# Optimization experiments

Hardware: AMD Instinct MI355X
Metric: run time of the kernel (lower is better)

## Reference

```python
import jax, jax.numpy as jnp
import numpy as np

CODEBOOK_SIZE = 8192
TOKEN_SIZE = 256
COMMITMENT_COST = 0.25


def setup_inputs() -> dict:
    key = jax.random.key(0)
    k1, k2 = jax.random.split(key)
    z = jax.random.normal(k1, (32, 1024, TOKEN_SIZE), dtype=jnp.float32)
    # embedding initialized uniform in [-1/K, 1/K] as in torch module
    embedding = jax.random.uniform(
        k2, (CODEBOOK_SIZE, TOKEN_SIZE), dtype=jnp.float32,
        minval=-1.0 / CODEBOOK_SIZE, maxval=1.0 / CODEBOOK_SIZE)
    return {"z": z, "embedding": embedding}


def reference(z, embedding):
    B, T, D = z.shape
    zf = z.reshape(B * T, D)                               # [N, D]
    # squared euclidean distances: ||z||^2 + ||e||^2 - 2 z.e
    d = (jnp.sum(zf * zf, axis=1, keepdims=True)
         + jnp.sum(embedding * embedding, axis=1)
         - 2.0 * jnp.einsum('nd,kd->nk', zf, embedding))   # [N, K]
    idx = jnp.argmin(d, axis=1)                            # [N]
    z_q = embedding[idx].reshape(B, T, D)                  # codebook gather
    commitment_loss = COMMITMENT_COST * jnp.mean(
        (jax.lax.stop_gradient(z_q) - z) ** 2)
    codebook_loss = jnp.mean((z_q - jax.lax.stop_gradient(z)) ** 2)
    loss = commitment_loss + codebook_loss                 # ema_update=False
    # straight-through estimator
    z_q_st = z + jax.lax.stop_gradient(z_q - z)
    return (z_q_st, loss, commitment_loss, codebook_loss,
            idx.reshape(B, T))
```

## Files before the change

kernel.cpp:

```cpp
#include <hip/hip_runtime.h>
#include <cfloat>

#define N_TOK   32768
#define K_CODES 8192
#define D_DIM   256
#define BTOK    128
#define CHUNK   128
#define NSPLIT  4
#define SPLITK  (K_CODES / NSPLIT)
#define CTAU_M  3.0e-5f
#define CAND_MM 2.4e-5f
#define MAXCAND 16
#define RBTOK   32
#define NRS     8
#define RSPLIT  (K_CODES / NRS)

typedef __attribute__((ext_vector_type(4)))  short bf16x4;
typedef __attribute__((ext_vector_type(8)))  short bf16x8;
typedef __attribute__((ext_vector_type(16))) float f32x16;


__device__ __forceinline__ float np_sumsq256(const float* __restrict__ row) {
    #pragma clang fp contract(off)
    float blk[2];
    #pragma unroll
    for (int b = 0; b < 2; b++) {
        const float* x = row + b * 128;
        float r[8];
        #pragma unroll
        for (int j = 0; j < 8; j++) { float v = x[j]; r[j] = v * v; }
        for (int i = 8; i < 128; i += 8) {
            #pragma unroll
            for (int j = 0; j < 8; j++) { float v = x[i + j]; r[j] += v * v; }
        }
        blk[b] = ((r[0] + r[1]) + (r[2] + r[3])) + ((r[4] + r[5]) + (r[6] + r[7]));
    }
    return blk[0] + blk[1];
}

__device__ __forceinline__ float np_einsum256(const float* __restrict__ a,
                                              const float* __restrict__ b) {
    #pragma clang fp contract(off)
    float A0 = 0.f, A1 = 0.f, A2 = 0.f, A3 = 0.f;
    for (int m = 0; m < 256; m += 16) {
        A0 = a[m+ 0]*b[m+ 0] + (a[m+ 4]*b[m+ 4] + (a[m+ 8]*b[m+ 8] + (a[m+12]*b[m+12] + A0)));
        A1 = a[m+ 1]*b[m+ 1] + (a[m+ 5]*b[m+ 5] + (a[m+ 9]*b[m+ 9] + (a[m+13]*b[m+13] + A1)));
        A2 = a[m+ 2]*b[m+ 2] + (a[m+ 6]*b[m+ 6] + (a[m+10]*b[m+10] + (a[m+14]*b[m+14] + A2)));
        A3 = a[m+ 3]*b[m+ 3] + (a[m+ 7]*b[m+ 7] + (a[m+11]*b[m+11] + (a[m+15]*b[m+15] + A3)));
    }
    return (A0 + A1) + (A2 + A3);
}

__device__ __forceinline__ float np_dtilde(float Cn, float e2k, float g) {
    #pragma clang fp contract(off)
    float t = Cn + e2k;
    float d = t - 2.0f * g;
    return d;
}

__device__ __forceinline__ unsigned short bf16_rne(float f) {
    unsigned u = __float_as_uint(f);
    unsigned r = u + 0x7fffu + ((u >> 16) & 1u);
    return (unsigned short)(r >> 16);
}
__device__ __forceinline__ void split_bf16(float f, short& hi, short& lo) {
    unsigned short h = bf16_rne(f);
    hi = (short)h;
    float hf = __uint_as_float(((unsigned)h) << 16);
    lo = (short)bf16_rne(f - hf);
}
__device__ __forceinline__ bf16x8 lo8(bf16x8 h, float4 a, float4 b) {
    float f[8] = {a.x, a.y, a.z, a.w, b.x, b.y, b.z, b.w};
    bf16x8 r;
    #pragma unroll
    for (int i = 0; i < 8; i++) {
        float hf = __uint_as_float(((unsigned)(unsigned short)h[i]) << 16);
        r[i] = (short)bf16_rne(f[i] - hf);
    }
    return r;
}

#define MFMA3(A, ah, al, bh, bl) \
    A = __builtin_amdgcn_mfma_f32_32x32x16_bf16(ah, bh, A, 0, 0, 0); \
    A = __builtin_amdgcn_mfma_f32_32x32x16_bf16(ah, bl, A, 0, 0, 0); \
    A = __builtin_amdgcn_mfma_f32_32x32x16_bf16(al, bh, A, 0, 0, 0);

__global__ __launch_bounds__(256) void prep_e_kernel(
    const float* __restrict__ emb, float* __restrict__ e2np,
    float* __restrict__ e2h, unsigned* __restrict__ ccount,
    double* __restrict__ loss_sum)
{
    int k = blockIdx.x * 256 + threadIdx.x;
    float v = np_sumsq256(emb + (size_t)k * D_DIM);
    e2np[k] = v;
    e2h[k]  = 0.5f * v;
    if (k == 0) { *ccount = 0u; *loss_sum = 0.0; }
}

__global__ __launch_bounds__(256) void prep_z_kernel(
    const float* __restrict__ z, float* __restrict__ Cnp)
{
    int t = blockIdx.x * 256 + threadIdx.x;
    Cnp[t] = np_sumsq256(z + (size_t)t * D_DIM);
}

__global__ __launch_bounds__(256) void cvt_e_kernel(
    const float* __restrict__ src, short* __restrict__ hi, short* __restrict__ lo)
{
    size_t p = ((size_t)blockIdx.x * 256 + threadIdx.x) * 8;
    float4 v0 = *(const float4*)(src + p);
    float4 v1 = *(const float4*)(src + p + 4);
    short h[8], l[8];
    split_bf16(v0.x, h[0], l[0]); split_bf16(v0.y, h[1], l[1]);
    split_bf16(v0.z, h[2], l[2]); split_bf16(v0.w, h[3], l[3]);
    split_bf16(v1.x, h[4], l[4]); split_bf16(v1.y, h[5], l[5]);
    split_bf16(v1.z, h[6], l[6]); split_bf16(v1.w, h[7], l[7]);
    bf16x8 vh = {h[0],h[1],h[2],h[3],h[4],h[5],h[6],h[7]};
    bf16x8 vl = {l[0],l[1],l[2],l[3],l[4],l[5],l[6],l[7]};
    *(bf16x8*)(hi + p) = vh;
    *(bf16x8*)(lo + p) = vl;
}

__global__ __launch_bounds__(256) void cvt_zhi_kernel(
    const float* __restrict__ src, short* __restrict__ hi)
{
    size_t p = ((size_t)blockIdx.x * 256 + threadIdx.x) * 8;
    float4 v0 = *(const float4*)(src + p);
    float4 v1 = *(const float4*)(src + p + 4);
    bf16x8 vh = {(short)bf16_rne(v0.x), (short)bf16_rne(v0.y),
                 (short)bf16_rne(v0.z), (short)bf16_rne(v0.w),
                 (short)bf16_rne(v1.x), (short)bf16_rne(v1.y),
                 (short)bf16_rne(v1.z), (short)bf16_rne(v1.w)};
    *(bf16x8*)(hi + p) = vh;
}

#define B_ESH 0
#define B_ESL 4096
#define B_ZSH 8192
#define B_ZSL 12288
#define TILE1 1024

__global__ __launch_bounds__(256, 3) void bulk_kernel(
    const float* __restrict__ zf, const short* __restrict__ zhi,
    const short* __restrict__ ehi, const short* __restrict__ elo,
    const float* __restrict__ e2h,
    float* __restrict__ m1a, float* __restrict__ m2a, int* __restrict__ i1a)
{
    __shared__ __align__(16) short smem[16384];
    __shared__ float e2s[CHUNK];
    __shared__ float s1m[BTOK], s2m[BTOK];
    __shared__ int   i1m[BTOK];

    const int tid  = threadIdx.x;
    const int lane = tid & 63;
    const int w    = tid >> 6;
    const int wt   = w & 1, wc = w >> 1;
    const int g     = blockIdx.x & 255;
    const int split = blockIdx.x >> 8;
    const int tok0  = g * BTOK;
    const int cs0   = split * SPLITK;

    const int r0 = tid >> 2, q0 = tid & 3;
    const int r1 = r0 + 64;
    const int so0 = r0 * 32 + ((q0 ^ ((r0 >> 1) & 3)) << 3);
    const int so1 = r1 * 32 + ((q0 ^ ((r1 >> 1) & 3)) << 3);

    const int l31 = lane & 31, hh = lane >> 5;
    const int swz = (l31 >> 1) & 3;
    const int arow = (wc * 64 + l31) * 32;
    const int brow = (wt * 64 + l31) * 32;
    const int a0 = arow + ((hh ^ swz) << 3);
    const int a1 = arow + (((2 + hh) ^ swz) << 3);
    const int b0 = brow + ((hh ^ swz) << 3);
    const int b1 = brow + (((2 + hh) ^ swz) << 3);

    float m1[2] = {-FLT_MAX, -FLT_MAX}, m2[2] = {-FLT_MAX, -FLT_MAX};
    int   k1[2] = {0x7fffffff, 0x7fffffff};

    for (int c = 0; c < SPLITK / CHUNK; c++) {
        const int code0 = cs0 + c * CHUNK;
        const float e2v = (tid < CHUNK) ? e2h[code0 + tid] : 0.f;
        f32x16 acc[2][2];
        #pragma unroll
        for (int i = 0; i < 2; i++)
            #pragma unroll
            for (int j = 0; j < 2; j++)
                #pragma unroll
                for (int r = 0; r < 16; r++) acc[i][j][r] = 0.f;

        for (int st = 0; st < 8; st++) {
            const int d0 = st * 32;
            const size_t ei0 = ((size_t)(code0 + r0) << 8) + d0 + (q0 << 3);
            const size_t ei1 = ((size_t)(code0 + r1) << 8) + d0 + (q0 << 3);
            const size_t zi0 = ((size_t)(tok0 + r0) << 8) + d0 + (q0 << 3);
            const size_t zi1 = ((size_t)(tok0 + r1) << 8) + d0 + (q0 << 3);
            bf16x8 eh0 = *(const bf16x8*)(ehi + ei0);
            bf16x8 el0 = *(const bf16x8*)(elo + ei0);
            bf16x8 eh1 = *(const bf16x8*)(ehi + ei1);
            bf16x8 el1 = *(const bf16x8*)(elo + ei1);
            bf16x8 zh0 = *(const bf16x8*)(zhi + zi0);
            bf16x8 zh1 = *(const bf16x8*)(zhi + zi1);
            float4 zf0a = *(const float4*)(zf + zi0);
            float4 zf0b = *(const float4*)(zf + zi0 + 4);
            float4 zf1a = *(const float4*)(zf + zi1);
            float4 zf1b = *(const float4*)(zf + zi1 + 4);
            bf16x8 zl0 = lo8(zh0, zf0a, zf0b);
            bf16x8 zl1 = lo8(zh1, zf1a, zf1b);
            __syncthreads();
            *(bf16x8*)(smem + B_ESH + so0) = eh0;
            *(bf16x8*)(smem + B_ESL + so0) = el0;
            *(bf16x8*)(smem + B_ESH + so1) = eh1;
            *(bf16x8*)(smem + B_ESL + so1) = el1;
            *(bf16x8*)(smem + B_ZSH + so0) = zh0;
            *(bf16x8*)(smem + B_ZSL + so0) = zl0;
            *(bf16x8*)(smem + B_ZSH + so1) = zh1;
            *(bf16x8*)(smem + B_ZSL + so1) = zl1;
            if (st == 0 && tid < CHUNK) e2s[tid] = e2v;
            __syncthreads();
            {
                bf16x8 a0h = *(const bf16x8*)(smem + B_ESH + a0);
                bf16x8 a0l = *(const bf16x8*)(smem + B_ESL + a0);
                bf16x8 a1h = *(const bf16x8*)(smem + B_ESH + TILE1 + a0);
                bf16x8 a1l = *(const bf16x8*)(smem + B_ESL + TILE1 + a0);
                bf16x8 b0h = *(const bf16x8*)(smem + B_ZSH + b0);
                bf16x8 b0l = *(const bf16x8*)(smem + B_ZSL + b0);
                bf16x8 b1h = *(const bf16x8*)(smem + B_ZSH + TILE1 + b0);
                bf16x8 b1l = *(const bf16x8*)(smem + B_ZSL + TILE1 + b0);
                MFMA3(acc[0][0], a0h, a0l, b0h, b0l);
                MFMA3(acc[0][1], a0h, a0l, b1h, b1l);
                MFMA3(acc[1][0], a1h, a1l, b0h, b0l);
                MFMA3(acc[1][1], a1h, a1l, b1h, b1l);
            }
            {
                bf16x8 a0h = *(const bf16x8*)(smem + B_ESH + a1);
                bf16x8 a0l = *(const bf16x8*)(smem + B_ESL + a1);
                bf16x8 a1h = *(const bf16x8*)(smem + B_ESH + TILE1 + a1);
                bf16x8 a1l = *(const bf16x8*)(smem + B_ESL + TILE1 + a1);
                bf16x8 b0h = *(const bf16x8*)(smem + B_ZSH + b1);
                bf16x8 b0l = *(const bf16x8*)(smem + B_ZSL + b1);
                bf16x8 b1h = *(const bf16x8*)(smem + B_ZSH + TILE1 + b1);
                bf16x8 b1l = *(const bf16x8*)(smem + B_ZSL + TILE1 + b1);
                MFMA3(acc[0][0], a0h, a0l, b0h, b0l);
                MFMA3(acc[0][1], a0h, a0l, b1h, b1l);
                MFMA3(acc[1][0], a1h, a1l, b0h, b0l);
                MFMA3(acc[1][1], a1h, a1l, b1h, b1l);
            }
        }
        #pragma unroll
        for (int tc = 0; tc < 2; tc++) {
            float ev[16];
            #pragma unroll
            for (int r = 0; r < 16; r++)
                ev[r] = e2s[wc * 64 + tc * 32 + hh * 4 + (r & 3) + ((r >> 2) << 3)];
            #pragma unroll
            for (int tt = 0; tt < 2; tt++) {
                #pragma unroll
                for (int r = 0; r < 16; r++) {
                    float a = acc[tc][tt][r] - ev[r];
                    int code = code0 + wc * 64 + tc * 32 + hh * 4 + (r & 3) + ((r >> 2) << 3);
                    if (a > m1[tt]) { m2[tt] = m1[tt]; m1[tt] = a; k1[tt] = code; }
                    else if (a > m2[tt]) m2[tt] = a;
                }
            }
        }
    }

    #pragma unroll
    for (int tt = 0; tt < 2; tt++) {
        float o1 = __shfl_xor(m1[tt], 32);
        float o2 = __shfl_xor(m2[tt], 32);
        int   oi = __shfl_xor(k1[tt], 32);
        bool take = (o1 > m1[tt]) || (o1 == m1[tt] && oi < k1[tt]);
        float w1 = take ? o1 : m1[tt];
        int   wi = take ? oi : k1[tt];
        float ls = take ? m1[tt] : o1;
        m2[tt] = fmaxf(fmaxf(m2[tt], o2), ls);
        m1[tt] = w1; k1[tt] = wi;
    }
    __syncthreads();
    if (wc == 0 && lane < 32) {
        #pragma unroll
        for (int tt = 0; tt < 2; tt++) {
            int tl = wt * 64 + tt * 32 + lane;
            s1m[tl] = m1[tt]; s2m[tl] = m2[tt]; i1m[tl] = k1[tt];
        }
    }
    __syncthreads();
    if (wc == 1 && lane < 32) {
        #pragma unroll
        for (int tt = 0; tt < 2; tt++) {
            int tl = wt * 64 + tt * 32 + lane;
            float a1 = s1m[tl], a2 = s2m[tl]; int ai = i1m[tl];
            bool take = (a1 > m1[tt]) || (a1 == m1[tt] && ai < k1[tt]);
            float w1 = take ? a1 : m1[tt];
            int   wi = take ? ai : k1[tt];
            float ls = take ? m1[tt] : a1;
            float w2 = fmaxf(fmaxf(m2[tt], a2), ls);
            size_t t = (size_t)(tok0 + tl) * NSPLIT + split;
            m1a[t] = w1; m2a[t] = w2; i1a[t] = wi;
        }
    }
}

__global__ __launch_bounds__(256) void merge_kernel(
    const float* __restrict__ m1a, const float* __restrict__ m2a,
    const int* __restrict__ i1a, float* __restrict__ m1f,
    int* __restrict__ idxf, int* __restrict__ clist,
    unsigned* __restrict__ ccount, unsigned* __restrict__ ccnt_g)
{
    int t = blockIdx.x * 256 + threadIdx.x;
    ccnt_g[t] = 0u;
    float w1 = m1a[t * NSPLIT], w2 = m2a[t * NSPLIT];
    int   wi = i1a[t * NSPLIT];
    #pragma unroll
    for (int s = 1; s < NSPLIT; s++) {
        float a1 = m1a[t * NSPLIT + s], a2 = m2a[t * NSPLIT + s];
        int   ai = i1a[t * NSPLIT + s];
        bool take = (a1 > w1) || (a1 == w1 && ai < wi);
        float n1 = take ? a1 : w1;
        int   ni = take ? ai : wi;
        float ls = take ? w1 : a1;
        w2 = fmaxf(fmaxf(w2, a2), ls);
        w1 = n1; wi = ni;
    }
    idxf[t] = wi; m1f[t] = w1;
    if (w1 - w2 < CTAU_M) {
        unsigned p = atomicAdd(ccount, 1u);
        clist[p] = t;
    }
}

#define R_ESH 0
#define R_ESL 4096
#define R_ZSH 8192
#define R_ZSL 9216

__global__ __launch_bounds__(256) void rescue_kernel(
    const float* __restrict__ zf, const short* __restrict__ zhi,
    const short* __restrict__ ehi, const short* __restrict__ elo,
    const float* __restrict__ e2h, const float* __restrict__ m1f,
    const unsigned* __restrict__ ccount, const int* __restrict__ clist,
    unsigned* __restrict__ ccnt_g, int* __restrict__ cand_g)
{
    const unsigned count = *ccount;
    const unsigned base  = blockIdx.x * RBTOK;
    if (base >= count) return;
    const int nt = min(RBTOK, (int)(count - base));
    const int sp = blockIdx.y;

    __shared__ __align__(16) short rsm[10240];
    __shared__ int   tls[RBTOK];
    __shared__ float thr[RBTOK];
    __shared__ float e2s[CHUNK];

    const int tid  = threadIdx.x;
    const int lane = tid & 63;
    const int w    = tid >> 6;

    if (tid < RBTOK) {
        int s = (tid < nt) ? tid : (nt - 1);
        int t = clist[base + s];
        tls[tid] = t;
        thr[tid] = (tid < nt) ? (m1f[t] - CAND_MM) : FLT_MAX;
    }
    __syncthreads();

    const int l31 = lane & 31, hh = lane >> 5;
    const float mythr = thr[l31];
    const int   mytok = tls[l31];
    const int swz = (l31 >> 1) & 3;
    const int arow = (w * 32 + l31) * 32;
    const int brow = l31 * 32;
    const int a0 = arow + ((hh ^ swz) << 3);
    const int a1 = arow + (((2 + hh) ^ swz) << 3);
    const int b0 = brow + ((hh ^ swz) << 3);
    const int b1 = brow + (((2 + hh) ^ swz) << 3);

    const int er0 = tid >> 2, eq0 = tid & 3;
    const int er1 = er0 + 64;
    const int eso0 = er0 * 32 + ((eq0 ^ ((er0 >> 1) & 3)) << 3);
    const int eso1 = er1 * 32 + ((eq0 ^ ((er1 >> 1) & 3)) << 3);
    const int zr = (tid & 127) >> 2, zq = tid & 3;
    const int zso = zr * 32 + ((zq ^ ((zr >> 1) & 3)) << 3);

    for (int c = 0; c < RSPLIT / CHUNK; c++) {
        const int code0 = sp * RSPLIT + c * CHUNK;
        const float e2v = (tid < CHUNK) ? e2h[code0 + tid] : 0.f;
        f32x16 acc;
        #pragma unroll
        for (int r = 0; r < 16; r++) acc[r] = 0.f;

        for (int st = 0; st < 8; st++) {
            const int d0 = st * 32;
            const size_t ei0 = ((size_t)(code0 + er0) << 8) + d0 + (eq0 << 3);
            const size_t ei1 = ((size_t)(code0 + er1) << 8) + d0 + (eq0 << 3);
            bf16x8 eh0 = *(const bf16x8*)(ehi + ei0);
            bf16x8 el0 = *(const bf16x8*)(elo + ei0);
            bf16x8 eh1 = *(const bf16x8*)(ehi + ei1);
            bf16x8 el1 = *(const bf16x8*)(elo + ei1);
            bf16x8 zh = {}, zl = {};
            if (tid < 128) {
                const size_t zi = ((size_t)tls[zr] << 8) + d0 + (zq << 3);
                zh = *(const bf16x8*)(zhi + zi);
                float4 za = *(const float4*)(zf + zi);
                float4 zb = *(const float4*)(zf + zi + 4);
                zl = lo8(zh, za, zb);
            }
            __syncthreads();
            *(bf16x8*)(rsm + R_ESH + eso0) = eh0;
            *(bf16x8*)(rsm + R_ESL + eso0) = el0;
            *(bf16x8*)(rsm + R_ESH + eso1) = eh1;
            *(bf16x8*)(rsm + R_ESL + eso1) = el1;
            if (tid < 128) {
                *(bf16x8*)(rsm + R_ZSH + zso) = zh;
                *(bf16x8*)(rsm + R_ZSL + zso) = zl;
            }
            if (st == 0 && tid < CHUNK) e2s[tid] = e2v;
            __syncthreads();
            {
                bf16x8 ah = *(const bf16x8*)(rsm + R_ESH + a0);
                bf16x8 al = *(const bf16x8*)(rsm + R_ESL + a0);
                bf16x8 bh = *(const bf16x8*)(rsm + R_ZSH + b0);
                bf16x8 bl = *(const bf16x8*)(rsm + R_ZSL + b0);
                MFMA3(acc, ah, al, bh, bl);
            }
            {
                bf16x8 ah = *(const bf16x8*)(rsm + R_ESH + a1);
                bf16x8 al = *(const bf16x8*)(rsm + R_ESL + a1);
                bf16x8 bh = *(const bf16x8*)(rsm + R_ZSH + b1);
                bf16x8 bl = *(const bf16x8*)(rsm + R_ZSL + b1);
                MFMA3(acc, ah, al, bh, bl);
            }
        }
        #pragma unroll
        for (int r = 0; r < 16; r++) {
            const int local = w * 32 + hh * 4 + (r & 3) + ((r >> 2) << 3);
            float a = acc[r] - e2s[local];
            if (a >= mythr) {
                unsigned p = atomicAdd(&ccnt_g[mytok], 1u);
                if (p < MAXCAND) cand_g[(size_t)mytok * MAXCAND + p] = code0 + local;
            }
        }
    }
}

__global__ __launch_bounds__(256) void resolve_kernel(
    const float* __restrict__ z, const float* __restrict__ emb,
    const float* __restrict__ e2np, const float* __restrict__ Cnp,
    const unsigned* __restrict__ ccount, const int* __restrict__ clist,
    const unsigned* __restrict__ ccnt_g, const int* __restrict__ cand_g,
    int* __restrict__ idxf)
{
    const unsigned count = *ccount;
    const int lane = threadIdx.x & 63;
    const int w    = threadIdx.x >> 6;
    for (unsigned c = blockIdx.x * 4 + w; c < count; c += gridDim.x * 4) {
        const int t = clist[c];
        const int n = (int)min(ccnt_g[t], (unsigned)MAXCAND);
        float bd = FLT_MAX; int bk = 0x7fffffff;
        if (lane < n) {
            const int k = cand_g[(size_t)t * MAXCAND + lane];
            float g = np_einsum256(z + (size_t)t * D_DIM, emb + (size_t)k * D_DIM);
            bd = np_dtilde(Cnp[t], e2np[k], g);
            bk = k;
        }
        #pragma unroll
        for (int off = 32; off >= 1; off >>= 1) {
            float od = __shfl_xor(bd, off);
            int   ok = __shfl_xor(bk, off);
            if (od < bd || (od == bd && ok < bk)) { bd = od; bk = ok; }
        }
        if (lane == 0 && n > 0) idxf[t] = bk;
    }
}

__global__ __launch_bounds__(256) void out_loss_kernel(
    const float* __restrict__ z, const float* __restrict__ emb,
    const int* __restrict__ idxf, float* __restrict__ out0,
    double* __restrict__ loss_sum)
{
    const int total4 = N_TOK * (D_DIM / 4);
    double lsum = 0.0;
    for (int p = blockIdx.x * 256 + threadIdx.x; p < total4; p += gridDim.x * 256) {
        const int n  = p >> 6;
        const int d4 = p & 63;
        const int k  = idxf[n];
        float4 zv = ((const float4*)z)[p];
        float4 ev = ((const float4*)(emb + (size_t)k * D_DIM))[d4];
        float dx = ev.x - zv.x, dy = ev.y - zv.y,
              dz = ev.z - zv.z, dw = ev.w - zv.w;
        float4 o;
        o.x = zv.x + dx; o.y = zv.y + dy; o.z = zv.z + dz; o.w = zv.w + dw;
        ((float4*)out0)[p] = o;
        lsum += (double)dx * dx + (double)dy * dy
              + (double)dz * dz + (double)dw * dw;
    }
    #pragma unroll
    for (int off = 32; off >= 1; off >>= 1) lsum += __shfl_xor(lsum, off);
    __shared__ double wsum[4];
    const int wv = threadIdx.x >> 6;
    if ((threadIdx.x & 63) == 0) wsum[wv] = lsum;
    __syncthreads();
    if (threadIdx.x == 0)
        atomicAdd(loss_sum, wsum[0] + wsum[1] + wsum[2] + wsum[3]);
}

__global__ __launch_bounds__(256) void finalize_kernel(
    const int* __restrict__ idxf, const double* __restrict__ loss_sum,
    float* __restrict__ out)
{
    const int t = blockIdx.x * 256 + threadIdx.x;
    if (t < N_TOK) out[8388611 + t] = (float)idxf[t];
    if (t == 0) {
        double mse = *loss_sum * (1.0 / 8388608.0);
        out[8388608] = (float)(1.25 * mse);
        out[8388609] = (float)(0.25 * mse);
        out[8388610] = (float)mse;
    }
}

extern "C" void kernel_launch(void* const* d_in, const int* in_sizes, int n_in,
                              void* d_out, int out_size, void* d_ws, size_t ws_size,
                              hipStream_t stream)
{
    const float* z   = (const float*)d_in[0];
    const float* emb = (const float*)d_in[1];
    float* out = (float*)d_out;
    char*  ws  = (char*)d_ws;
    char*  ob  = (char*)d_out;

    short*    ehi    = (short*)(ob + 0);
    short*    elo    = (short*)(ob + 4194304);
    short*    zhi    = (short*)(ob + 8388608);
    float*    m1a    = (float*)(ob + 25165824);
    float*    m2a    = (float*)(ob + 25690112);
    int*      i1a    = (int*)(ob + 26214400);
    int*      cand_g = (int*)(ob + 26738688);

    double*   loss_sum = (double*)(ws + 0);
    unsigned* ccount   = (unsigned*)(ws + 8);
    float*    e2np     = (float*)(ws + 16);
    float*    e2h      = (float*)(ws + 32784);
    float*    Cnp      = (float*)(ws + 65552);
    float*    m1f      = (float*)(ws + 196624);
    int*      idxf     = (int*)(ws + 327696);
    int*      clist    = (int*)(ws + 458768);
    unsigned* ccnt_g   = (unsigned*)(ws + 589840);

    prep_e_kernel<<<dim3(K_CODES / 256), dim3(256), 0, stream>>>(
        emb, e2np, e2h, ccount, loss_sum);
    prep_z_kernel<<<dim3(N_TOK / 256), dim3(256), 0, stream>>>(z, Cnp);
    cvt_e_kernel<<<dim3(K_CODES * D_DIM / 8 / 256), dim3(256), 0, stream>>>(emb, ehi, elo);
    cvt_zhi_kernel<<<dim3(N_TOK * D_DIM / 8 / 256), dim3(256), 0, stream>>>(z, zhi);
    bulk_kernel<<<dim3((N_TOK / BTOK) * NSPLIT), dim3(256), 0, stream>>>(
        z, zhi, ehi, elo, e2h, m1a, m2a, i1a);
    merge_kernel<<<dim3(N_TOK / 256), dim3(256), 0, stream>>>(
        m1a, m2a, i1a, m1f, idxf, clist, ccount, ccnt_g);
    rescue_kernel<<<dim3(N_TOK / RBTOK, NRS), dim3(256), 0, stream>>>(
        z, zhi, ehi, elo, e2h, m1f, ccount, clist, ccnt_g, cand_g);
    resolve_kernel<<<dim3(128), dim3(256), 0, stream>>>(
        z, emb, e2np, Cnp, ccount, clist, ccnt_g, cand_g, idxf);
    out_loss_kernel<<<dim3(1024), dim3(256), 0, stream>>>(
        z, emb, idxf, out, loss_sum);
    finalize_kernel<<<dim3(N_TOK / 256), dim3(256), 0, stream>>>(
        idxf, loss_sum, out);
}
```

Measured before the change: 923.9 us.

## Double-buffer LDS tiles with register prefetch in bulk distance kernel

```diff
diff --git a/kernel.cpp b/kernel.cpp
--- a/kernel.cpp
+++ b/kernel.cpp
@@ -1,4 +1,5 @@
 #include <hip/hip_runtime.h>
+#include <hip/hip_bf16.h>
 #include <cfloat>
 
 #define N_TOK   32768
@@ -73,9 +74,13 @@
     float f[8] = {a.x, a.y, a.z, a.w, b.x, b.y, b.z, b.w};
     bf16x8 r;
     #pragma unroll
-    for (int i = 0; i < 8; i++) {
-        float hf = __uint_as_float(((unsigned)(unsigned short)h[i]) << 16);
-        r[i] = (short)bf16_rne(f[i] - hf);
+    for (int i = 0; i < 8; i += 2) {
+        float d0 = f[i]     - __uint_as_float(((unsigned)(unsigned short)h[i])     << 16);
+        float d1 = f[i + 1] - __uint_as_float(((unsigned)(unsigned short)h[i + 1]) << 16);
+        __hip_bfloat162 p = __float22bfloat162_rn(make_float2(d0, d1));
+        unsigned u; __builtin_memcpy(&u, &p, 4);
+        r[i]     = (short)(u & 0xffffu);
+        r[i + 1] = (short)(u >> 16);
     }
     return r;
 }
@@ -140,14 +145,14 @@
 #define B_ZSL 12288
 #define TILE1 1024
 
-__global__ __launch_bounds__(256, 3) void bulk_kernel(
+__global__ __launch_bounds__(256, 2) void bulk_kernel(
     const float* __restrict__ zf, const short* __restrict__ zhi,
     const short* __restrict__ ehi, const short* __restrict__ elo,
     const float* __restrict__ e2h,
     float* __restrict__ m1a, float* __restrict__ m2a, int* __restrict__ i1a)
 {
-    __shared__ __align__(16) short smem[16384];
-    __shared__ float e2s[CHUNK];
+    __shared__ __align__(16) short smem[2][16384];
+    __shared__ float e2s[2][CHUNK];
     __shared__ float s1m[BTOK], s2m[BTOK];
     __shared__ int   i1m[BTOK];
 
@@ -177,92 +182,125 @@
     float m1[2] = {-FLT_MAX, -FLT_MAX}, m2[2] = {-FLT_MAX, -FLT_MAX};
     int   k1[2] = {0x7fffffff, 0x7fffffff};
 
-    for (int c = 0; c < SPLITK / CHUNK; c++) {
+    bf16x8 eh0p, el0p, eh1p, el1p, zh0p, zh1p;
+    float4 zf0ap, zf0bp, zf1ap, zf1bp;
+    float  e2vp = 0.f;
+
+    f32x16 acc[2][2];
+    #pragma unroll
+    for (int i = 0; i < 2; i++)
+        #pragma unroll
+        for (int j = 0; j < 2; j++)
+            #pragma unroll
+            for (int r = 0; r < 16; r++) acc[i][j][r] = 0.f;
+
+    const int NST = (SPLITK / CHUNK) * 8;
+
+    auto ISSUE = [&](int s) {
+        const int c  = s >> 3;
+        const int st = s & 7;
         const int code0 = cs0 + c * CHUNK;
-        const float e2v = (tid < CHUNK) ? e2h[code0 + tid] : 0.f;
-        f32x16 acc[2][2];
-        #pragma unroll
-        for (int i = 0; i < 2; i++)
-            #pragma unroll
-            for (int j = 0; j < 2; j++)
-                #pragma unroll
-                for (int r = 0; r < 16; r++) acc[i][j][r] = 0.f;
-
-        for (int st = 0; st < 8; st++) {
-            const int d0 = st * 32;
-            const size_t ei0 = ((size_t)(code0 + r0) << 8) + d0 + (q0 << 3);
-            const size_t ei1 = ((size_t)(code0 + r1) << 8) + d0 + (q0 << 3);
-            const size_t zi0 = ((size_t)(tok0 + r0) << 8) + d0 + (q0 << 3);
-            const size_t zi1 = ((size_t)(tok0 + r1) << 8) + d0 + (q0 << 3);
-            bf16x8 eh0 = *(const bf16x8*)(ehi + ei0);
-            bf16x8 el0 = *(const bf16x8*)(elo + ei0);
-            bf16x8 eh1 = *(const bf16x8*)(ehi + ei1);
-            bf16x8 el1 = *(const bf16x8*)(elo + ei1);
-            bf16x8 zh0 = *(const bf16x8*)(zhi + zi0);
-            bf16x8 zh1 = *(const bf16x8*)(zhi + zi1);
-            float4 zf0a = *(const float4*)(zf + zi0);
-            float4 zf0b = *(const float4*)(zf + zi0 + 4);
-            float4 zf1a = *(const float4*)(zf + zi1);
-            float4 zf1b = *(const float4*)(zf + zi1 + 4);
-            bf16x8 zl0 = lo8(zh0, zf0a, zf0b);
-            bf16x8 zl1 = lo8(zh1, zf1a, zf1b);
-            __syncthreads();
-            *(bf16x8*)(smem + B_ESH + so0) = eh0;
-            *(bf16x8*)(smem + B_ESL + so0) = el0;
-            *(bf16x8*)(smem + B_ESH + so1) = eh1;
-            *(bf16x8*)(smem + B_ESL + so1) = el1;
-            *(bf16x8*)(smem + B_ZSH + so0) = zh0;
-            *(bf16x8*)(smem + B_ZSL + so0) = zl0;
-            *(bf16x8*)(smem + B_ZSH + so1) = zh1;
-            *(bf16x8*)(smem + B_ZSL + so1) = zl1;
-            if (st == 0 && tid < CHUNK) e2s[tid] = e2v;
-            __syncthreads();
+        const int d0 = st * 32;
+        const size_t ei0 = ((size_t)(code0 + r0) << 8) + d0 + (q0 << 3);
+        const size_t ei1 = ((size_t)(code0 + r1) << 8) + d0 + (q0 << 3);
+        const size_t zi0 = ((size_t)(tok0 + r0) << 8) + d0 + (q0 << 3);
+        const size_t zi1 = ((size_t)(tok0 + r1) << 8) + d0 + (q0 << 3);
+        eh0p = *(const bf16x8*)(ehi + ei0);
+        el0p = *(const bf16x8*)(elo + ei0);
+        eh1p = *(const bf16x8*)(ehi + ei1);
+        el1p = *(const bf16x8*)(elo + ei1);
+        zh0p = *(const bf16x8*)(zhi + zi0);
+        zh1p = *(const bf16x8*)(zhi + zi1);
+        zf0ap = *(const float4*)(zf + zi0);
+        zf0bp = *(const float4*)(zf + zi0 + 4);
+        zf1ap = *(const float4*)(zf + zi1);
+        zf1bp = *(const float4*)(zf + zi1 + 4);
+        if (st == 0 && tid < CHUNK) e2vp = e2h[code0 + tid];
+    };
+
+    auto STORE = [&](int buf, int s) {
+        bf16x8 zl0 = lo8(zh0p, zf0ap, zf0bp);
+        bf16x8 zl1 = lo8(zh1p, zf1ap, zf1bp);
+        short* sm = smem[buf];
+        *(bf16x8*)(sm + B_ESH + so0) = eh0p;
+        *(bf16x8*)(sm + B_ESL + so0) = el0p;
+        *(bf16x8*)(sm + B_ESH + so1) = eh1p;
+        *(bf16x8*)(sm + B_ESL + so1) = el1p;
+        *(bf16x8*)(sm + B_ZSH + so0) = zh0p;
+        *(bf16x8*)(sm + B_ZSL + so0) = zl0;
+        *(bf16x8*)(sm + B_ZSH + so1) = zh1p;
+        *(bf16x8*)(sm + B_ZSL + so1) = zl1;
+        if ((s & 7) == 0 && tid < CHUNK) e2s[(s >> 3) & 1][tid] = e2vp;
+    };
+
+    ISSUE(0);
+    STORE(0, 0);
+    __syncthreads();
+
+    #pragma unroll 2
+    for (int s = 0; s < NST; s++) {
+        const int cur = s & 1;
+        if (s + 1 < NST) ISSUE(s + 1);
+        {
+            const short* sm = smem[cur];
             {
-                bf16x8 a0h = *(const bf16x8*)(smem + B_ESH + a0);
-                bf16x8 a0l = *(const bf16x8*)(smem + B_ESL + a0);
-                bf16x8 a1h = *(const bf16x8*)(smem + B_ESH + TILE1 + a0);
-                bf16x8 a1l = *(const bf16x8*)(smem + B_ESL + TILE1 + a0);
-                bf16x8 b0h = *(const bf16x8*)(smem + B_ZSH + b0);
-                bf16x8 b0l = *(const bf16x8*)(smem + B_ZSL + b0);
-                bf16x8 b1h = *(const bf16x8*)(smem + B_ZSH + TILE1 + b0);
-                bf16x8 b1l = *(const bf16x8*)(smem + B_ZSL + TILE1 + b0);
+                bf16x8 a0h = *(const bf16x8*)(sm + B_ESH + a0);
+                bf16x8 a0l = *(const bf16x8*)(sm + B_ESL + a0);
+                bf16x8 a1h = *(const bf16x8*)(sm + B_ESH + TILE1 + a0);
+                bf16x8 a1l = *(const bf16x8*)(sm + B_ESL + TILE1 + a0);
+                bf16x8 b0h = *(const bf16x8*)(sm + B_ZSH + b0);
+                bf16x8 b0l = *(const bf16x8*)(sm + B_ZSL + b0);
+                bf16x8 b1h = *(const bf16x8*)(sm + B_ZSH + TILE1 + b0);
+                bf16x8 b1l = *(const bf16x8*)(sm + B_ZSL + TILE1 + b0);
                 MFMA3(acc[0][0], a0h, a0l, b0h, b0l);
                 MFMA3(acc[0][1], a0h, a0l, b1h, b1l);
                 MFMA3(acc[1][0], a1h, a1l, b0h, b0l);
                 MFMA3(acc[1][1], a1h, a1l, b1h, b1l);
             }
             {
-                bf16x8 a0h = *(const bf16x8*)(smem + B_ESH + a1);
-                bf16x8 a0l = *(const bf16x8*)(smem + B_ESL + a1);
-                bf16x8 a1h = *(const bf16x8*)(smem + B_ESH + TILE1 + a1);
-                bf16x8 a1l = *(const bf16x8*)(smem + B_ESL + TILE1 + a1);
-                bf16x8 b0h = *(const bf16x8*)(smem + B_ZSH + b1);
-                bf16x8 b0l = *(const bf16x8*)(smem + B_ZSL + b1);
-                bf16x8 b1h = *(const bf16x8*)(smem + B_ZSH + TILE1 + b1);
-                bf16x8 b1l = *(const bf16x8*)(smem + B_ZSL + TILE1 + b1);
+                bf16x8 a0h = *(const bf16x8*)(sm + B_ESH + a1);
+                bf16x8 a0l = *(const bf16x8*)(sm + B_ESL + a1);
+                bf16x8 a1h = *(const bf16x8*)(sm + B_ESH + TILE1 + a1);
+                bf16x8 a1l = *(const bf16x8*)(sm + B_ESL + TILE1 + a1);
+                bf16x8 b0h = *(const bf16x8*)(sm + B_ZSH + b1);
+                bf16x8 b0l = *(const bf16x8*)(sm + B_ZSL + b1);
+                bf16x8 b1h = *(const bf16x8*)(sm + B_ZSH + TILE1 + b1);
+                bf16x8 b1l = *(const bf16x8*)(sm + B_ZSL + TILE1 + b1);
                 MFMA3(acc[0][0], a0h, a0l, b0h, b0l);
                 MFMA3(acc[0][1], a0h, a0l, b1h, b1l);
                 MFMA3(acc[1][0], a1h, a1l, b0h, b0l);
                 MFMA3(acc[1][1], a1h, a1l, b1h, b1l);
             }
         }
-        #pragma unroll
-        for (int tc = 0; tc < 2; tc++) {
-            float ev[16];
+        if ((s & 7) == 7) {
+            const int code0 = cs0 + (s >> 3) * CHUNK;
+            const float* e2c = e2s[(s >> 3) & 1];
             #pragma unroll
-            for (int r = 0; r < 16; r++)
-                ev[r] = e2s[wc * 64 + tc * 32 + hh * 4 + (r & 3) + ((r >> 2) << 3)];
+            for (int tc = 0; tc < 2; tc++) {
+                float ev[16];
+                #pragma unroll
+                for (int r = 0; r < 16; r++)
+                    ev[r] = e2c[wc * 64 + tc * 32 + hh * 4 + (r & 3) + ((r >> 2) << 3)];
+                #pragma unroll
+                for (int tt = 0; tt < 2; tt++) {
+                    #pragma unroll
+                    for (int r = 0; r < 16; r++) {
+                        float a = acc[tc][tt][r] - ev[r];
+                        int code = code0 + wc * 64 + tc * 32 + hh * 4 + (r & 3) + ((r >> 2) << 3);
+                        if (a > m1[tt]) { m2[tt] = m1[tt]; m1[tt] = a; k1[tt] = code; }
+                        else if (a > m2[tt]) m2[tt] = a;
+                    }
+                }
+            }
             #pragma unroll
-            for (int tt = 0; tt < 2; tt++) {
+            for (int i = 0; i < 2; i++)
                 #pragma unroll
-                for (int r = 0; r < 16; r++) {
-                    float a = acc[tc][tt][r] - ev[r];
-                    int code = code0 + wc * 64 + tc * 32 + hh * 4 + (r & 3) + ((r >> 2) << 3);
-                    if (a > m1[tt]) { m2[tt] = m1[tt]; m1[tt] = a; k1[tt] = code; }
-                    else if (a > m2[tt]) m2[tt] = a;
-                }
-            }
-        }
+                for (int j = 0; j < 2; j++)
+                    #pragma unroll
+                    for (int r = 0; r < 16; r++) acc[i][j][r] = 0.f;
+        }
+        if (s + 1 < NST) STORE(cur ^ 1, s + 1);
+        __syncthreads();
     }
 
     #pragma unroll
```

New measurement: 802.0 us. -13.2%, faster.
